# Kernel tuning notes

Measured on AMD Instinct MI355X. Metric: run time of the kernel, lower is better.

Reference implementation:

```python
import jax, jax.numpy as jnp
import numpy as np

B, C = 8192, 10000

def setup_inputs() -> dict:
    key = jax.random.key(0)
    k1, k2, k3 = jax.random.split(key, 3)
    x = jax.random.normal(k1, (B, C), dtype=jnp.float32)
    target = jax.random.randint(k2, (B,), 0, C)
    # soft-label matrix: rows are probability distributions (as produced by update())
    matrix = jax.nn.softmax(jax.random.normal(k3, (C, C), dtype=jnp.float32), axis=-1)
    grad_state = jnp.zeros((C, C), dtype=jnp.float32)
    count = jnp.zeros((C, 1), dtype=jnp.float32)
    return {"x": x, "target": target, "matrix": matrix, "grad_state": grad_state, "count": count}

def reference(x, target, matrix, grad_state, count):
    target = target.reshape(-1)
    logprobs = jax.nn.log_softmax(x, axis=-1)          # [B, C]
    softlabel = matrix[target]                          # gather rows: [B, C]
    loss = jnp.mean(jnp.sum(-softlabel * logprobs, axis=-1))  # reduction='mean'
    # training-branch statistics (detached in original)
    p = jax.nn.softmax(jax.lax.stop_gradient(x), axis=-1)
    pred = jnp.argmax(p, axis=-1)
    correct = (pred == target)                          # [B] bool
    # scatter-add correct probs into per-class rows (replaces python Counter loop)
    add = jax.ops.segment_sum(p * correct[:, None].astype(p.dtype), target, num_segments=C)
    cnt = jax.ops.segment_sum(correct.astype(jnp.float32), target, num_segments=C)[:, None]
    new_grad = grad_state + add
    new_count = count + cnt
    return loss, new_grad, new_count
```

## Files before the change

### kernel.cpp

```cpp
#include <hip/hip_runtime.h>

#define CLS 10000
#define BATCH 8192
#define NGRAD 100000000LL

typedef float v4f __attribute__((ext_vector_type(4)));

#define ROW_BLOCKS BATCH
#define N4 ((NGRAD - 4) / 4)
#define COPY_PER_THREAD 4
#define COPY_CHUNK (256 * COPY_PER_THREAD)
#define COPY_BLOCKS ((int)((N4 + COPY_CHUNK - 1) / COPY_CHUNK))

__device__ __forceinline__ void combine_ms(float& m, float& s, float om, float os) {
  float nm = fmaxf(m, om);
  s = s * __expf(m - nm) + os * __expf(om - nm);
  m = nm;
}

__global__ __launch_bounds__(256) void fused_main(
    const float* __restrict__ x, const int* __restrict__ target,
    const float* __restrict__ matrix, const float* __restrict__ grad_state,
    const float* __restrict__ count, float* __restrict__ out,
    float* __restrict__ row_loss, float* __restrict__ row_logZ,
    int* __restrict__ row_correct)
{
  int blk = blockIdx.x;

  if (blk == ROW_BLOCKS) {
    float* out_count = out + 1 + NGRAD;
    for (int c = threadIdx.x; c < CLS; c += 256) out_count[c] = count[c];
    if (threadIdx.x == 0) {
      out[1] = grad_state[0];
      out[2] = grad_state[1];
      out[3] = grad_state[2];
      out[NGRAD] = grad_state[NGRAD - 1];
    }
    return;
  }

  if (blk > ROW_BLOCKS) {
    long long base = (long long)(blk - (ROW_BLOCKS + 1)) * COPY_CHUNK + threadIdx.x;
    const float* src = grad_state + 3;
    v4f* dst = (v4f*)(out + 4);
#pragma unroll
    for (int j = 0; j < COPY_PER_THREAD; ++j) {
      long long k = base + (long long)j * 256;
      if (k < N4) {
        const float* s = src + 4 * k;
        v4f v;
        v[0] = __builtin_nontemporal_load(s + 0);
        v[1] = __builtin_nontemporal_load(s + 1);
        v[2] = __builtin_nontemporal_load(s + 2);
        v[3] = __builtin_nontemporal_load(s + 3);
        __builtin_nontemporal_store(v, dst + k);
      }
    }
    return;
  }

  int b = blk;
  int t = target[b];
  const v4f* xr = (const v4f*)(x + (size_t)b * CLS);
  const float4* mr = (const float4*)(matrix + (size_t)t * CLS);

  float m = -3.4e38f, s = 0.f, dot = 0.f;
  float bestv = -3.4e38f;
  int besti = 0x7fffffff;

  for (int i = threadIdx.x; i < CLS / 4; i += 256) {
    v4f xv = __builtin_nontemporal_load(xr + i);
    float4 mv = mr[i];
    dot += xv[0] * mv.x;
    dot += xv[1] * mv.y;
    dot += xv[2] * mv.z;
    dot += xv[3] * mv.w;
    float vals[4] = {xv[0], xv[1], xv[2], xv[3]};
#pragma unroll
    for (int j = 0; j < 4; ++j) {
      float v = vals[j];
      int idx = 4 * i + j;
      if (v > bestv || (v == bestv && idx < besti)) { bestv = v; besti = idx; }
      float nm = fmaxf(m, v);
      s = s * __expf(m - nm) + __expf(v - nm);
      m = nm;
    }
  }

#pragma unroll
  for (int off = 32; off > 0; off >>= 1) {
    float om = __shfl_down(m, off);
    float os = __shfl_down(s, off);
    float od = __shfl_down(dot, off);
    float ov = __shfl_down(bestv, off);
    int   oi = __shfl_down(besti, off);
    combine_ms(m, s, om, os);
    dot += od;
    if (ov > bestv || (ov == bestv && oi < besti)) { bestv = ov; besti = oi; }
  }

  __shared__ float sm[4], ss[4], sd[4], sv[4];
  __shared__ int si[4];
  int wave = threadIdx.x >> 6;
  if ((threadIdx.x & 63) == 0) {
    sm[wave] = m; ss[wave] = s; sd[wave] = dot; sv[wave] = bestv; si[wave] = besti;
  }
  __syncthreads();
  if (threadIdx.x == 0) {
    for (int w = 1; w < 4; ++w) {
      combine_ms(m, s, sm[w], ss[w]);
      dot += sd[w];
      if (sv[w] > bestv || (sv[w] == bestv && si[w] < besti)) { bestv = sv[w]; besti = si[w]; }
    }
    float logZ = m + __logf(s);
    row_logZ[b] = logZ;
    row_correct[b] = (besti == t) ? 1 : 0;
    row_loss[b] = logZ - dot;
  }
}

__global__ __launch_bounds__(256) void fused_epilogue(
    const float* __restrict__ x, const int* __restrict__ target,
    const float* __restrict__ row_loss, const float* __restrict__ row_logZ,
    const int* __restrict__ row_correct, float* __restrict__ out)
{
  int b = blockIdx.x;

  if (b == 0) {
    float acc = 0.f;
    for (int i = threadIdx.x; i < BATCH; i += 256) acc += row_loss[i];
#pragma unroll
    for (int off = 32; off > 0; off >>= 1) acc += __shfl_down(acc, off);
    __shared__ float sw[4];
    if ((threadIdx.x & 63) == 0) sw[threadIdx.x >> 6] = acc;
    __syncthreads();
    if (threadIdx.x == 0)
      out[0] = (sw[0] + sw[1] + sw[2] + sw[3]) * (1.0f / BATCH);
  }

  if (!row_correct[b]) return;
  int t = target[b];
  float lz = row_logZ[b];
  const float* xr = x + (size_t)b * CLS;
  float* gr = out + 1 + (size_t)t * CLS;
  float* out_count = out + 1 + NGRAD;
  for (int c = threadIdx.x; c < CLS; c += 256)
    atomicAdd(&gr[c], __expf(xr[c] - lz));
  if (threadIdx.x == 0) atomicAdd(&out_count[t], 1.0f);
}

extern "C" void kernel_launch(void* const* d_in, const int* in_sizes, int n_in,
                              void* d_out, int out_size, void* d_ws, size_t ws_size,
                              hipStream_t stream)
{
  const float* x          = (const float*)d_in[0];
  const int*   target     = (const int*)d_in[1];
  const float* matrix     = (const float*)d_in[2];
  const float* grad_state = (const float*)d_in[3];
  const float* count      = (const float*)d_in[4];

  float* out = (float*)d_out;

  float* row_loss    = (float*)d_ws;
  float* row_logZ    = row_loss + BATCH;
  int*   row_correct = (int*)(row_logZ + BATCH);

  int gridA = ROW_BLOCKS + 1 + COPY_BLOCKS;
  fused_main<<<gridA, 256, 0, stream>>>(x, target, matrix, grad_state, count,
                                        out, row_loss, row_logZ, row_correct);
  fused_epilogue<<<BATCH, 256, 0, stream>>>(x, target, row_loss, row_logZ,
                                            row_correct, out);
}
```

Baseline: 1.049 ms.

## Interleave row and copy blocks; replace online softmax with register-held two-pass

Row-reduction blocks are interleaved with grad-state copy blocks (one row block per three copy blocks), so compute-bound and bandwidth-bound work run together on the GPU instead of all copy blocks queuing after the row blocks. The per-row pass keeps the x values in registers, finds the max with the argmax, then computes the sum of exponentials in a second pass. This removes the online rescaling exp per element. It costs more registers and an extra block barrier.

```diff
diff --git a/kernel.cpp b/kernel.cpp
--- a/kernel.cpp
+++ b/kernel.cpp
@@ -11,12 +11,8 @@
 #define COPY_PER_THREAD 4
 #define COPY_CHUNK (256 * COPY_PER_THREAD)
 #define COPY_BLOCKS ((int)((N4 + COPY_CHUNK - 1) / COPY_CHUNK))
-
-__device__ __forceinline__ void combine_ms(float& m, float& s, float om, float os) {
-  float nm = fmaxf(m, om);
-  s = s * __expf(m - nm) + os * __expf(om - nm);
-  m = nm;
-}
+#define GRID_MAIN (4 * ROW_BLOCKS + 1)
+#define NQ 10
 
 __global__ __launch_bounds__(256) void fused_main(
     const float* __restrict__ x, const int* __restrict__ target,
@@ -27,7 +23,7 @@
 {
   int blk = blockIdx.x;
 
-  if (blk == ROW_BLOCKS) {
+  if (blk == 4 * ROW_BLOCKS) {
     float* out_count = out + 1 + NGRAD;
     for (int c = threadIdx.x; c < CLS; c += 256) out_count[c] = count[c];
     if (threadIdx.x == 0) {
@@ -39,8 +35,11 @@
     return;
   }
 
-  if (blk > ROW_BLOCKS) {
-    long long base = (long long)(blk - (ROW_BLOCKS + 1)) * COPY_CHUNK + threadIdx.x;
+  int r = blk & 3;
+  if (r != 0) {
+    long long copyId = (long long)(blk >> 2) * 3 + (r - 1);
+    if (copyId >= COPY_BLOCKS) return;
+    long long base = copyId * (long long)COPY_CHUNK + threadIdx.x;
     const float* src = grad_state + 3;
     v4f* dst = (v4f*)(out + 4);
 #pragma unroll
@@ -59,63 +58,84 @@
     return;
   }
 
-  int b = blk;
+  int b = blk >> 2;
   int t = target[b];
   const v4f* xr = (const v4f*)(x + (size_t)b * CLS);
-  const float4* mr = (const float4*)(matrix + (size_t)t * CLS);
+  const v4f* mr = (const v4f*)(matrix + (size_t)t * CLS);
 
-  float m = -3.4e38f, s = 0.f, dot = 0.f;
+  v4f xs[NQ];
+  float d0 = 0.f, d1 = 0.f, d2 = 0.f, d3 = 0.f;
   float bestv = -3.4e38f;
   int besti = 0x7fffffff;
 
-  for (int i = threadIdx.x; i < CLS / 4; i += 256) {
-    v4f xv = __builtin_nontemporal_load(xr + i);
-    float4 mv = mr[i];
-    dot += xv[0] * mv.x;
-    dot += xv[1] * mv.y;
-    dot += xv[2] * mv.z;
-    dot += xv[3] * mv.w;
-    float vals[4] = {xv[0], xv[1], xv[2], xv[3]};
 #pragma unroll
-    for (int j = 0; j < 4; ++j) {
-      float v = vals[j];
-      int idx = 4 * i + j;
-      if (v > bestv || (v == bestv && idx < besti)) { bestv = v; besti = idx; }
-      float nm = fmaxf(m, v);
-      s = s * __expf(m - nm) + __expf(v - nm);
-      m = nm;
+  for (int k = 0; k < NQ; ++k) {
+    int i = threadIdx.x + k * 256;
+    if (i < CLS / 4) {
+      v4f xv = __builtin_nontemporal_load(xr + i);
+      v4f mv = mr[i];
+      xs[k] = xv;
+      d0 += xv[0] * mv[0];
+      d1 += xv[1] * mv[1];
+      d2 += xv[2] * mv[2];
+      d3 += xv[3] * mv[3];
+#pragma unroll
+      for (int j = 0; j < 4; ++j) {
+        float v = xv[j];
+        int idx = 4 * i + j;
+        if (v > bestv || (v == bestv && idx < besti)) { bestv = v; besti = idx; }
+      }
+    } else {
+      xs[k] = (v4f){-3.4e38f, -3.4e38f, -3.4e38f, -3.4e38f};
     }
   }
+  float dot = (d0 + d1) + (d2 + d3);
 
 #pragma unroll
   for (int off = 32; off > 0; off >>= 1) {
-    float om = __shfl_down(m, off);
-    float os = __shfl_down(s, off);
-    float od = __shfl_down(dot, off);
     float ov = __shfl_down(bestv, off);
     int   oi = __shfl_down(besti, off);
-    combine_ms(m, s, om, os);
+    float od = __shfl_down(dot, off);
     dot += od;
     if (ov > bestv || (ov == bestv && oi < besti)) { bestv = ov; besti = oi; }
   }
 
-  __shared__ float sm[4], ss[4], sd[4], sv[4];
-  __shared__ int si[4];
+  __shared__ float sv[4], sd[4], ssum[4];
+  __shared__ int si_[4];
+  __shared__ float sM, sDot;
+  __shared__ int sBest;
   int wave = threadIdx.x >> 6;
-  if ((threadIdx.x & 63) == 0) {
-    sm[wave] = m; ss[wave] = s; sd[wave] = dot; sv[wave] = bestv; si[wave] = besti;
-  }
+  if ((threadIdx.x & 63) == 0) { sv[wave] = bestv; si_[wave] = besti; sd[wave] = dot; }
   __syncthreads();
   if (threadIdx.x == 0) {
     for (int w = 1; w < 4; ++w) {
-      combine_ms(m, s, sm[w], ss[w]);
       dot += sd[w];
-      if (sv[w] > bestv || (sv[w] == bestv && si[w] < besti)) { bestv = sv[w]; besti = si[w]; }
+      if (sv[w] > bestv || (sv[w] == bestv && si_[w] < besti)) { bestv = sv[w]; besti = si_[w]; }
     }
-    float logZ = m + __logf(s);
+    sM = bestv; sBest = besti; sDot = dot;
+  }
+  __syncthreads();
+  float M = sM;
+
+  float s0 = 0.f, s1 = 0.f, s2 = 0.f, s3 = 0.f;
+#pragma unroll
+  for (int k = 0; k < NQ; ++k) {
+    s0 += __expf(xs[k][0] - M);
+    s1 += __expf(xs[k][1] - M);
+    s2 += __expf(xs[k][2] - M);
+    s3 += __expf(xs[k][3] - M);
+  }
+  float s = (s0 + s1) + (s2 + s3);
+#pragma unroll
+  for (int off = 32; off > 0; off >>= 1) s += __shfl_down(s, off);
+  if ((threadIdx.x & 63) == 0) ssum[wave] = s;
+  __syncthreads();
+  if (threadIdx.x == 0) {
+    float S = ssum[0] + ssum[1] + ssum[2] + ssum[3];
+    float logZ = M + __logf(S);
     row_logZ[b] = logZ;
-    row_correct[b] = (besti == t) ? 1 : 0;
-    row_loss[b] = logZ - dot;
+    row_correct[b] = (sBest == t) ? 1 : 0;
+    row_loss[b] = logZ - sDot;
   }
 }
 
@@ -165,9 +185,8 @@
   float* row_logZ    = row_loss + BATCH;
   int*   row_correct = (int*)(row_logZ + BATCH);
 
-  int gridA = ROW_BLOCKS + 1 + COPY_BLOCKS;
-  fused_main<<<gridA, 256, 0, stream>>>(x, target, matrix, grad_state, count,
-                                        out, row_loss, row_logZ, row_correct);
+  fused_main<<<GRID_MAIN, 256, 0, stream>>>(x, target, matrix, grad_state, count,
+                                            out, row_loss, row_logZ, row_correct);
   fused_epilogue<<<BATCH, 256, 0, stream>>>(x, target, row_loss, row_logZ,
                                             row_correct, out);
 }
```

Result: slower. 1.116 ms (+6.3%).
